# Kernel tuning notes

Hardware: AMD Instinct MI355X
Metric: run time of the kernel (lower is better)

## Reference

```python
import jax, jax.numpy as jnp
import numpy as np

D_MODEL = 1024
D_STATE = 8          # max(8, 16 // 2)
D_CONV = 4
D_INNER = int(1.5 * D_MODEL)   # expand = max(1.5, 2*0.75)
DT_RANK = (D_MODEL + 15) // 16 # 64
D_FF = 2 * D_MODEL
B, L = 2, 2048


def layer_norm(x, g, b, eps=1e-5):
    mu = jnp.mean(x, -1, keepdims=True)
    var = jnp.var(x, -1, keepdims=True)
    return (x - mu) * jax.lax.rsqrt(var + eps) * g + b


def setup_inputs() -> dict:
    key = jax.random.key(0)
    ks = jax.random.split(key, 12)
    def n(k, shape, scale=0.02):
        return jax.random.normal(k, shape, dtype=jnp.float32) * scale
    return {
        'x': jax.random.normal(ks[0], (B, L, D_MODEL), dtype=jnp.float32),
        'ln1_g': jnp.ones((D_MODEL,), jnp.float32),
        'ln1_b': jnp.zeros((D_MODEL,), jnp.float32),
        'ln2_g': jnp.ones((D_MODEL,), jnp.float32),
        'ln2_b': jnp.zeros((D_MODEL,), jnp.float32),
        'in_proj_w': n(ks[1], (2 * D_INNER, D_MODEL)),
        'conv_w': n(ks[2], (D_INNER, 1, D_CONV), 0.1),
        'conv_b': jnp.zeros((D_INNER,), jnp.float32),
        'x_proj_w': n(ks[3], (DT_RANK + 2 * D_STATE, D_INNER)),
        'dt_proj_w': n(ks[4], (D_INNER, DT_RANK), 0.1),
        'dt_proj_b': n(ks[5], (D_INNER,), 0.1),
        'A_log': jnp.log(jnp.broadcast_to(jnp.arange(1, D_STATE + 1, dtype=jnp.float32), (D_INNER, D_STATE))),
        'D': jnp.ones((D_INNER,), jnp.float32),
        'out_proj_w': n(ks[6], (D_MODEL, D_INNER)),
        'ffn_w1': n(ks[7], (D_FF, D_MODEL)),
        'ffn_b1': jnp.zeros((D_FF,), jnp.float32),
        'ffn_w2': n(ks[8], (D_MODEL, D_FF)),
        'ffn_b2': jnp.zeros((D_MODEL,), jnp.float32),
    }


def mamba(x, in_proj_w, conv_w, conv_b, x_proj_w, dt_proj_w, dt_proj_b, A_log, Dp, out_proj_w):
    # in_proj -> (x, z)
    xz = x @ in_proj_w.T                       # (B, L, 2*d_inner)
    xi, z = jnp.split(xz, 2, axis=-1)
    # depthwise causal conv over seq, kernel 4
    xc = jnp.transpose(xi, (0, 2, 1))          # (B, d_inner, L)
    xc = jax.lax.conv_general_dilated(
        xc, conv_w, window_strides=(1,), padding=[(D_CONV - 1, 0)],
        dimension_numbers=('NCH', 'OIH', 'NCH'), feature_group_count=D_INNER)
    xc = xc + conv_b[None, :, None]
    u = jax.nn.silu(jnp.transpose(xc, (0, 2, 1)))  # (B, L, d_inner)
    # x_proj -> dt, B, C
    x_dbl = u @ x_proj_w.T
    dt = x_dbl[..., :DT_RANK]
    Bm = x_dbl[..., DT_RANK:DT_RANK + D_STATE]
    Cm = x_dbl[..., DT_RANK + D_STATE:]
    delta = jax.nn.softplus(dt @ dt_proj_w.T + dt_proj_b)  # (B, L, d_inner)
    A = -jnp.exp(A_log)                                    # (d_inner, d_state)
    dA = jnp.exp(jnp.einsum('bld,dn->bldn', delta, A))     # (B, L, d_inner, d_state)
    dBu = jnp.einsum('bld,bln,bld->bldn', delta, Bm, u)
    # selective scan over time
    def step(h, inputs):
        dA_t, dBu_t, C_t = inputs
        h = dA_t * h + dBu_t                   # (B, d_inner, d_state)
        y = jnp.einsum('bdn,bn->bd', h, C_t)
        return h, y
    h0 = jnp.zeros((x.shape[0], D_INNER, D_STATE), x.dtype)
    _, ys = jax.lax.scan(step, h0, (jnp.moveaxis(dA, 1, 0), jnp.moveaxis(dBu, 1, 0), jnp.moveaxis(Cm, 1, 0)))
    y = jnp.moveaxis(ys, 0, 1) + u * Dp        # skip connection D*u
    y = y * jax.nn.silu(z)                     # gate
    return y @ out_proj_w.T


def reference(x, ln1_g, ln1_b, ln2_g, ln2_b, in_proj_w, conv_w, conv_b, x_proj_w,
              dt_proj_w, dt_proj_b, A_log, D, out_proj_w, ffn_w1, ffn_b1, ffn_w2, ffn_b2):
    residual = x
    xp = layer_norm(x, ln1_g, ln1_b)
    x = mamba(xp, in_proj_w, conv_w, conv_b, x_proj_w, dt_proj_w, dt_proj_b, A_log, D, out_proj_w) + residual
    xn = layer_norm(x, ln2_g, ln2_b)
    h = jax.nn.gelu(xn @ ffn_w1.T + ffn_b1, approximate=False)  # dropout is identity in eval
    return x + (h @ ffn_w2.T + ffn_b2)
```

## Files before the change

### kernel.cpp

```cpp
#include <hip/hip_runtime.h>
#include <math.h>

#define D_MODEL 1024
#define D_STATE 8
#define D_CONV  4
#define D_INNER 1536
#define DT_RANK 64
#define D_FF    2048
#define BATCH   2
#define SEQ     2048
#define NROWS   (BATCH*SEQ)
#define NC      32
#define LC      (SEQ/NC)
#define XPAD    128

typedef short bf16x8 __attribute__((ext_vector_type(8)));
typedef unsigned short u16x8 __attribute__((ext_vector_type(8)));
typedef float f32x4  __attribute__((ext_vector_type(4)));

__device__ inline unsigned short f2bf(float x) {
    union { float f; unsigned u; } v; v.f = x;
    unsigned r = v.u + 0x7fffu + ((v.u >> 16) & 1u);
    return (unsigned short)(r >> 16);
}
__device__ inline float bf2f(unsigned short h) {
    union { unsigned u; float f; } v; v.u = ((unsigned)h) << 16;
    return v.f;
}
__device__ inline float softplus_f(float x) {
    return (x > 20.0f) ? x : log1pf(__expf(x));
}
__device__ inline float gelu_f(float x) {
    return 0.5f * x * (1.0f + erff(x * 0.70710678118654752f));
}
__device__ inline float silu_f(float x) {
    return x / (1.0f + __expf(-x));
}
__device__ inline void gload16(const unsigned short* g, unsigned short* l) {
    typedef unsigned int u32;
    __builtin_amdgcn_global_load_lds(
        (const __attribute__((address_space(1))) u32*)g,
        (__attribute__((address_space(3))) u32*)l, 16, 0, 0);
}

#define PHASE_SYNC_PRE()  do { __builtin_amdgcn_s_barrier(); __builtin_amdgcn_sched_barrier(0); \
                               asm volatile("s_waitcnt lgkmcnt(0)" ::: "memory"); \
                               __builtin_amdgcn_sched_barrier(0); } while (0)
#define PHASE_SYNC_POST() do { __builtin_amdgcn_s_barrier(); __builtin_amdgcn_sched_barrier(0); } while (0)

__global__ __launch_bounds__(256) void wconv(const float* __restrict__ s0, unsigned short* __restrict__ d0,
                                             const float* __restrict__ s1, unsigned short* __restrict__ d1,
                                             const float* __restrict__ s2, unsigned short* __restrict__ d2,
                                             const float* __restrict__ s3, unsigned short* __restrict__ d3,
                                             const float* __restrict__ s4, unsigned short* __restrict__ d4) {
    int b = blockIdx.x;
    const float* s; unsigned short* d; int base;
    if      (b < 1536) { s = s0; d = d0; base = b * 2048; }
    else if (b < 1584) { s = s1; d = d1; base = (b - 1536) * 2048; }
    else if (b < 2352) { s = s2; d = d2; base = (b - 1584) * 2048; }
    else if (b < 3376) { s = s3; d = d3; base = (b - 2352) * 2048; }
    else               { s = s4; d = d4; base = (b - 3376) * 2048; }
    int i = base + threadIdx.x * 8;
    float4 v0 = *(const float4*)(s + i);
    float4 v1 = *(const float4*)(s + i + 4);
    ushort4 a, c;
    a.x = f2bf(v0.x); a.y = f2bf(v0.y); a.z = f2bf(v0.z); a.w = f2bf(v0.w);
    c.x = f2bf(v1.x); c.y = f2bf(v1.y); c.z = f2bf(v1.z); c.w = f2bf(v1.w);
    *(ushort4*)(d + i)     = a;
    *(ushort4*)(d + i + 4) = c;
}

__global__ __launch_bounds__(256) void xproj_pad(const float* __restrict__ src, unsigned short* __restrict__ dst) {
    int row = blockIdx.x;
    for (int c = threadIdx.x; c < D_INNER; c += 256)
        dst[row * D_INNER + c] = (row < 80) ? f2bf(src[row * D_INNER + c]) : (unsigned short)0;
}

__global__ __launch_bounds__(256) void ln_kernel(const float* __restrict__ x,
                                                 const float* __restrict__ g,
                                                 const float* __restrict__ b,
                                                 unsigned short* __restrict__ out) {
    __shared__ float sbuf[4];
    int row = blockIdx.x;
    int t = threadIdx.x;
    const float4* xr = (const float4*)(x + (size_t)row * D_MODEL);
    float4 v = xr[t];
    float s = v.x + v.y + v.z + v.w;
    for (int o = 32; o; o >>= 1) s += __shfl_down(s, o, 64);
    if ((t & 63) == 0) sbuf[t >> 6] = s;
    __syncthreads();
    float mu = (sbuf[0] + sbuf[1] + sbuf[2] + sbuf[3]) * (1.0f / D_MODEL);
    __syncthreads();
    float d0 = v.x - mu, d1 = v.y - mu, d2 = v.z - mu, d3 = v.w - mu;
    float q = d0*d0 + d1*d1 + d2*d2 + d3*d3;
    for (int o = 32; o; o >>= 1) q += __shfl_down(q, o, 64);
    if ((t & 63) == 0) sbuf[t >> 6] = q;
    __syncthreads();
    float var = (sbuf[0] + sbuf[1] + sbuf[2] + sbuf[3]) * (1.0f / D_MODEL);
    float rs = rsqrtf(var + 1e-5f);
    float4 gv = ((const float4*)g)[t];
    float4 bv = ((const float4*)b)[t];
    ushort4 st;
    st.x = f2bf(d0 * rs * gv.x + bv.x);
    st.y = f2bf(d1 * rs * gv.y + bv.y);
    st.z = f2bf(d2 * rs * gv.z + bv.z);
    st.w = f2bf(d3 * rs * gv.w + bv.w);
    ((ushort4*)(out + (size_t)row * D_MODEL))[t] = st;
}

#define EPI_F32        0
#define EPI_F32_BF16   1
#define EPI_SOFTPLUS   2
#define EPI_RESID      3
#define EPI_GELU_BF16  4
#define EPI_BIAS_RESID 5
#define EPI_BF16       6

template<int WN, int EPI>
__global__ __launch_bounds__(512, 2) void gemm8p(
    const unsigned short* __restrict__ A, int lda,
    const unsigned short* __restrict__ Bm, int ldb, int K,
    float* __restrict__ Cf, unsigned short* __restrict__ Cb, int ldc,
    const float* __restrict__ bias,
    const float* __restrict__ resid, int ldr) {
    constexpr int WM = 8 / WN;
    constexpr int BN = WN * 64;
    constexpr int RW = 256 / WM;
    constexpr int CW = 64;
    constexpr int MI = RW / 16;
    constexpr int NI = CW / 16;
    constexpr int MIH = MI / 2, NIH = NI / 2;
    constexpr int ABYTES = 256 * 128;
    constexpr int BBYTES = BN * 128;
    constexpr int BOFF = 2 * ABYTES;
    __shared__ unsigned short lds[(2 * ABYTES + 2 * BBYTES) / 2];

    const int t = threadIdx.x, l = t & 63, w = t >> 6;
    const int wr = w / WN, wc = w % WN;

    const int nx = gridDim.x;
    const int nwg = nx * gridDim.y;
    int bid = blockIdx.y * nx + blockIdx.x;
    int q = nwg >> 3;
    int swz = (bid & 7) * q + (bid >> 3);
    const int m0 = (swz / nx) * 256, n0 = (swz % nx) * BN;

    const int sr = l >> 3;
    const int sj = ((l & 7) * 16) ^ (((l >> 5) & 1) << 5);
    const int row_l = w * 8;
    const int row_c = (w >> 2) * 64 + (w & 3) * 8;

    auto STG = [&](int bufbyte, int rowbase, const unsigned short* G, int ldg, int gbase, int kt) {
        unsigned short* dst = (unsigned short*)((char*)lds + bufbyte + rowbase * 128);
        const unsigned short* src = G + (size_t)(gbase + rowbase + sr) * ldg + kt * 64 + (sj >> 1);
        gload16(src, dst);
    };
    auto S_Ah0 = [&](int b, int kt) {
        if (WN == 4) { STG(b * ABYTES, row_l, A, lda, m0, kt);       STG(b * ABYTES, 128 + row_l, A, lda, m0, kt); }
        else         { STG(b * ABYTES, row_c, A, lda, m0, kt);       STG(b * ABYTES, 128 + row_c, A, lda, m0, kt); }
    };
    auto S_Ah1 = [&](int b, int kt) {
        if (WN == 4) { STG(b * ABYTES, 64 + row_l, A, lda, m0, kt);  STG(b * ABYTES, 192 + row_l, A, lda, m0, kt); }
        else         { STG(b * ABYTES, 32 + row_c, A, lda, m0, kt);  STG(b * ABYTES, 160 + row_c, A, lda, m0, kt); }
    };
    auto S_Bc0 = [&](int b, int kt) {
        if (WN == 4) { STG(BOFF + b * BBYTES, row_c, Bm, ldb, n0, kt); STG(BOFF + b * BBYTES, 128 + row_c, Bm, ldb, n0, kt); }
        else         { STG(BOFF + b * BBYTES, row_c, Bm, ldb, n0, kt); }
    };
    auto S_Bc1 = [&](int b, int kt) {
        if (WN == 4) { STG(BOFF + b * BBYTES, 32 + row_c, Bm, ldb, n0, kt); STG(BOFF + b * BBYTES, 160 + row_c, Bm, ldb, n0, kt); }
        else         { STG(BOFF + b * BBYTES, 32 + row_c, Bm, ldb, n0, kt); }
    };

    auto LD = [&](int bytebase, int row, int kb) -> bf16x8 {
        int o = bytebase + row * 128 + (kb ^ (((row >> 2) & 1) << 5));
        return *(const bf16x8*)((const char*)lds + o);
    };

    f32x4 acc[MI][NI] = {};
    bf16x8 af[MIH][2], b0v[NIH][2], b1v[NIH][2];

    auto LDA_set = [&](int buf, int qr, auto& dst) {
        #pragma unroll
        for (int mi = 0; mi < MIH; mi++)
            #pragma unroll
            for (int ks = 0; ks < 2; ks++)
                dst[mi][ks] = LD(buf * ABYTES, wr * RW + qr * (RW / 2) + mi * 16 + (l & 15),
                                 ks * 64 + (l >> 4) * 16);
    };
    auto LDB_set = [&](int buf, int qc, auto& dst) {
        #pragma unroll
        for (int ni2 = 0; ni2 < NIH; ni2++)
            #pragma unroll
            for (int ks = 0; ks < 2; ks++)
                dst[ni2][ks] = LD(BOFF + buf * BBYTES, wc * CW + qc * 32 + ni2 * 16 + (l & 15),
                                  ks * 64 + (l >> 4) * 16);
    };
    auto MFMA_Q = [&](int qr, int qc, auto& a_, auto& b_) {
        __builtin_amdgcn_s_setprio(1);
        #pragma unroll
        for (int mi = 0; mi < MIH; mi++)
            #pragma unroll
            for (int ni2 = 0; ni2 < NIH; ni2++)
                #pragma unroll
                for (int ks = 0; ks < 2; ks++)
                    acc[qr * MIH + mi][qc * NIH + ni2] =
                        __builtin_amdgcn_mfma_f32_16x16x32_bf16(a_[mi][ks], b_[ni2][ks],
                                                                acc[qr * MIH + mi][qc * NIH + ni2], 0, 0, 0);
        __builtin_amdgcn_s_setprio(0);
    };
    auto VMW = [&](bool last) {
        if (last)            asm volatile("s_waitcnt vmcnt(0)" ::: "memory");
        else if (WN == 4)    asm volatile("s_waitcnt vmcnt(6)" ::: "memory");
        else                 asm volatile("s_waitcnt vmcnt(5)" ::: "memory");
        __builtin_amdgcn_sched_barrier(0);
    };

    const int ni_ = K >> 7;

    S_Ah0(0, 0); S_Ah1(0, 0); S_Bc0(0, 0); S_Bc1(0, 0);
    S_Ah0(1, 1); S_Ah1(1, 1); S_Bc0(1, 1); S_Bc1(1, 1);
    if (WN == 4) asm volatile("s_waitcnt vmcnt(8)" ::: "memory");
    else         asm volatile("s_waitcnt vmcnt(6)" ::: "memory");
    __builtin_amdgcn_s_barrier();
    __builtin_amdgcn_sched_barrier(0);

    for (int i = 0; i < ni_; i++) {
        const bool last = (i == ni_ - 1);
        const int t2 = 2 * i + 2, t3 = 2 * i + 3;
        LDA_set(0, 0, af); LDB_set(0, 0, b0v);
        if (i) S_Bc0(1, 2 * i + 1);
        PHASE_SYNC_PRE(); MFMA_Q(0, 0, af, b0v); PHASE_SYNC_POST();
        LDB_set(0, 1, b1v);
        if (!last) S_Ah0(0, t2);
        PHASE_SYNC_PRE(); MFMA_Q(0, 1, af, b1v); PHASE_SYNC_POST();
        LDA_set(0, 1, af);
        PHASE_SYNC_PRE(); MFMA_Q(1, 1, af, b1v); PHASE_SYNC_POST();
        LDB_set(0, 0, b0v);
        if (!last) { S_Ah1(0, t2); S_Bc1(0, t2); }
        VMW(last);
        PHASE_SYNC_PRE(); MFMA_Q(1, 0, af, b0v); PHASE_SYNC_POST();
        LDA_set(1, 0, af); LDB_set(1, 0, b0v);
        if (!last) S_Bc0(0, t2);
        PHASE_SYNC_PRE(); MFMA_Q(0, 0, af, b0v); PHASE_SYNC_POST();
        LDB_set(1, 1, b1v);
        if (!last) S_Ah0(1, t3);
        PHASE_SYNC_PRE(); MFMA_Q(0, 1, af, b1v); PHASE_SYNC_POST();
        LDA_set(1, 1, af);
        PHASE_SYNC_PRE(); MFMA_Q(1, 1, af, b1v); PHASE_SYNC_POST();
        LDB_set(1, 0, b0v);
        if (!last) { S_Ah1(1, t3); S_Bc1(1, t3); }
        VMW(last);
        PHASE_SYNC_PRE(); MFMA_Q(1, 0, af, b0v); PHASE_SYNC_POST();
    }

    #pragma unroll
    for (int ni2 = 0; ni2 < NI; ni2++) {
        int col = n0 + wc * CW + ni2 * 16 + (l & 15);
        float bv = 0.0f;
        if (EPI == EPI_SOFTPLUS || EPI == EPI_GELU_BF16 || EPI == EPI_BIAS_RESID) bv = bias[col];
        #pragma unroll
        for (int mi = 0; mi < MI; mi++) {
            #pragma unroll
            for (int j = 0; j < 4; j++) {
                int row = m0 + wr * RW + mi * 16 + (l >> 4) * 4 + j;
                float v = acc[mi][ni2][j];
                if (EPI == EPI_SOFTPLUS)        v = softplus_f(v + bv);
                else if (EPI == EPI_GELU_BF16)  v = gelu_f(v + bv);
                else if (EPI == EPI_RESID)      v = v + resid[(size_t)row * ldr + col];
                else if (EPI == EPI_BIAS_RESID) v = v + bv + resid[(size_t)row * ldr + col];
                if (EPI == EPI_GELU_BF16 || EPI == EPI_BF16) {
                    Cb[(size_t)row * ldc + col] = f2bf(v);
                } else {
                    Cf[(size_t)row * ldc + col] = v;
                    if (EPI == EPI_F32_BF16) Cb[(size_t)row * ldc + col] = f2bf(v);
                }
            }
        }
    }
}

template<int EPI, int SPLITK>
__global__ __launch_bounds__(256) void gemm_mfma(
    const unsigned short* __restrict__ A, int lda,
    const unsigned short* __restrict__ B, int ldb, int K,
    float* __restrict__ Cf, unsigned short* __restrict__ Cb, int ldc,
    const float* __restrict__ bias,
    const float* __restrict__ resid, int ldr) {
    __shared__ unsigned short As[3][128 * 32];
    __shared__ unsigned short Bs[3][128 * 32];
    int t = threadIdx.x, l = t & 63, w = t >> 6;
    int nx = gridDim.x;
    int nwg = nx * gridDim.y;
    int bid = blockIdx.y * nx + blockIdx.x;
    int q = nwg >> 3;
    int swz = (bid & 7) * q + (bid >> 3);
    int m0 = (swz / nx) * 128, n0 = (swz % nx) * 128;
    int kbase = (SPLITK > 1) ? blockIdx.z * K : 0;
    int c0 = 2 * w, c1 = 2 * w + 1;
    int srow = l >> 2, scol = (l & 3) * 8;
    const unsigned short* Ag0 = A + (size_t)(m0 + 16 * c0 + srow) * lda + kbase + scol;
    const unsigned short* Ag1 = A + (size_t)(m0 + 16 * c1 + srow) * lda + kbase + scol;
    const unsigned short* Bg0 = B + (size_t)(n0 + 16 * c0 + srow) * ldb + kbase + scol;
    const unsigned short* Bg1 = B + (size_t)(n0 + 16 * c1 + srow) * ldb + kbase + scol;
    int wr = w >> 1, wc = w & 1;
    int aoff = (wr * 64 + (l & 15)) * 32 + (l >> 4) * 8;
    int boff = (wc * 64 + (l & 15)) * 32 + (l >> 4) * 8;

    f32x4 acc[4][4] = {};
    int nt = K >> 5;

    gload16(Ag0, &As[0][c0 * 512]);
    gload16(Ag1, &As[0][c1 * 512]);
    gload16(Bg0, &Bs[0][c0 * 512]);
    gload16(Bg1, &Bs[0][c1 * 512]);
    if (nt > 1) {
        gload16(Ag0 + 32, &As[1][c0 * 512]);
        gload16(Ag1 + 32, &As[1][c1 * 512]);
        gload16(Bg0 + 32, &Bs[1][c0 * 512]);
        gload16(Bg1 + 32, &Bs[1][c1 * 512]);
    }

    int cur = 0;
    for (int ti = 0; ti < nt; ti++) {
        int pf = ti + 2;
        if (pf < nt) {
            int nb = cur - 1; if (nb < 0) nb += 3;
            int k0 = pf << 5;
            gload16(Ag0 + k0, &As[nb][c0 * 512]);
            gload16(Ag1 + k0, &As[nb][c1 * 512]);
            gload16(Bg0 + k0, &Bs[nb][c0 * 512]);
            gload16(Bg1 + k0, &Bs[nb][c1 * 512]);
        }
        int rem = nt - 1 - ti;
        if (rem >= 2)      asm volatile("s_waitcnt vmcnt(8)" ::: "memory");
        else if (rem == 1) asm volatile("s_waitcnt vmcnt(4)" ::: "memory");
        else               asm volatile("s_waitcnt vmcnt(0)" ::: "memory");
        __builtin_amdgcn_s_barrier();

        const unsigned short* Ab = &As[cur][0];
        const unsigned short* Bb = &Bs[cur][0];
        bf16x8 af[4], bfv[4];
        #pragma unroll
        for (int i = 0; i < 4; i++) af[i] = *(const bf16x8*)(Ab + aoff + i * 512);
        #pragma unroll
        for (int i = 0; i < 4; i++) bfv[i] = *(const bf16x8*)(Bb + boff + i * 512);
        __builtin_amdgcn_s_setprio(1);
        #pragma unroll
        for (int mi = 0; mi < 4; mi++)
            #pragma unroll
            for (int ni = 0; ni < 4; ni++)
                acc[mi][ni] = __builtin_amdgcn_mfma_f32_16x16x32_bf16(af[mi], bfv[ni], acc[mi][ni], 0, 0, 0);
        __builtin_amdgcn_s_setprio(0);
        __builtin_amdgcn_s_barrier();
        cur++; if (cur == 3) cur = 0;
    }

    if (SPLITK > 1) Cf += (size_t)blockIdx.z * NROWS * ldc;
    int colb = n0 + wc * 64 + (l & 15);
    int rowb = m0 + wr * 64 + (l >> 4) * 4;
    #pragma unroll
    for (int ni = 0; ni < 4; ni++) {
        int col = colb + ni * 16;
        float bv = 0.0f;
        if (EPI == EPI_SOFTPLUS || EPI == EPI_GELU_BF16 || EPI == EPI_BIAS_RESID) bv = bias[col];
        #pragma unroll
        for (int mi = 0; mi < 4; mi++) {
            #pragma unroll
            for (int j = 0; j < 4; j++) {
                int row = rowb + mi * 16 + j;
                float v = acc[mi][ni][j];
                if (EPI == EPI_SOFTPLUS)        v = softplus_f(v + bv);
                else if (EPI == EPI_GELU_BF16)  v = gelu_f(v + bv);
                else if (EPI == EPI_RESID)      v = v + resid[(size_t)row * ldr + col];
                else if (EPI == EPI_BIAS_RESID) v = v + bv + resid[(size_t)row * ldr + col];
                if (EPI == EPI_GELU_BF16 || EPI == EPI_BF16) {
                    Cb[(size_t)row * ldc + col] = f2bf(v);
                } else {
                    Cf[(size_t)row * ldc + col] = v;
                    if (EPI == EPI_F32_BF16) Cb[(size_t)row * ldc + col] = f2bf(v);
                }
            }
        }
    }
}

__global__ __launch_bounds__(256) void xdbl_reduce(const float* __restrict__ part,
                                                   float* __restrict__ xdbl,
                                                   unsigned short* __restrict__ xdbl_bf) {
    int i = blockIdx.x * 256 + threadIdx.x;
    const size_t seg = (size_t)NROWS * XPAD;
    float s = part[i] + part[i + seg] + part[i + 2 * seg] + part[i + 3 * seg];
    xdbl[i] = s;
    xdbl_bf[i] = f2bf(s);
}

__global__ __launch_bounds__(256) void conv_silu(const unsigned short* __restrict__ xz,
                                                 const float* __restrict__ w,
                                                 const float* __restrict__ cb,
                                                 unsigned short* __restrict__ u) {
    int idx = (blockIdx.x * 256 + threadIdx.x) * 8;
    int d = idx % D_INNER;
    int bl = idx / D_INNER;
    int l = bl & (SEQ - 1);
    float acc[8];
    float4 wv[8];
    #pragma unroll
    for (int j = 0; j < 8; j++) wv[j] = *(const float4*)(w + (d + j) * 4);
    float4 cb0 = *(const float4*)(cb + d);
    float4 cb1 = *(const float4*)(cb + d + 4);
    acc[0] = cb0.x; acc[1] = cb0.y; acc[2] = cb0.z; acc[3] = cb0.w;
    acc[4] = cb1.x; acc[5] = cb1.y; acc[6] = cb1.z; acc[7] = cb1.w;
    #pragma unroll
    for (int k = 0; k < 4; k++) {
        int lp = l - 3 + k;
        if (lp >= 0) {
            u16x8 s = *(const u16x8*)(xz + (size_t)(bl - 3 + k) * (2 * D_INNER) + d);
            #pragma unroll
            for (int j = 0; j < 8; j++) {
                float wk = (k == 0) ? wv[j].x : (k == 1) ? wv[j].y : (k == 2) ? wv[j].z : wv[j].w;
                acc[j] += bf2f((unsigned short)s[j]) * wk;
            }
        }
    }
    u16x8 o;
    #pragma unroll
    for (int j = 0; j < 8; j++) o[j] = f2bf(silu_f(acc[j]));
    *(u16x8*)(u + idx) = o;
}

__global__ __launch_bounds__(256) void scan_passA(const float* __restrict__ delta,
                                                  const unsigned short* __restrict__ u,
                                                  const float* __restrict__ xdbl,
                                                  const float* __restrict__ A_log,
                                                  float* __restrict__ P,
                                                  float* __restrict__ S) {
    int d = blockIdx.x * 256 + threadIdx.x;
    int c = blockIdx.y, b = blockIdx.z;
    __shared__ float bc[LC][16];
    int base_row = b * SEQ + c * LC;
    for (int e = threadIdx.x; e < LC * 16; e += 256) {
        int lrr = e >> 4, col = e & 15;
        bc[lrr][col] = xdbl[(size_t)(base_row + lrr) * XPAD + DT_RANK + col];
    }
    __syncthreads();
    float Ad[8];
    #pragma unroll
    for (int n = 0; n < 8; n++) Ad[n] = -__expf(A_log[d * 8 + n]);
    float prod[8], hs[8];
    #pragma unroll
    for (int n = 0; n < 8; n++) { prod[n] = 1.0f; hs[n] = 0.0f; }
    for (int lrr = 0; lrr < LC; lrr++) {
        int row = base_row + lrr;
        float dl = delta[(size_t)row * D_INNER + d];
        float uu = bf2f(u[(size_t)row * D_INNER + d]);
        float du = dl * uu;
        #pragma unroll
        for (int n = 0; n < 8; n++) {
            float dA = __expf(dl * Ad[n]);
            prod[n] *= dA;
            hs[n] = dA * hs[n] + du * bc[lrr][n];
        }
    }
    size_t o = ((size_t)((size_t)b * NC + c) * D_INNER + d) * 8;
    #pragma unroll
    for (int n = 0; n < 8; n++) { P[o + n] = prod[n]; S[o + n] = hs[n]; }
}

__global__ __launch_bounds__(256) void scan_passB(const float* __restrict__ P,
                                                  const float* __restrict__ S,
                                                  float* __restrict__ hstart) {
    int tid = blockIdx.x * 256 + threadIdx.x;
    int b = tid / (D_INNER * 8);
    int rem = tid % (D_INNER * 8);
    float h = 0.0f;
    for (int c = 0; c < NC; c++) {
        size_t o = (size_t)(b * NC + c) * (D_INNER * 8) + rem;
        hstart[o] = h;
        h = P[o] * h + S[o];
    }
}

__global__ __launch_bounds__(256) void scan_passC(const float* __restrict__ delta,
                                                  const unsigned short* __restrict__ u,
                                                  const float* __restrict__ xdbl,
                                                  const float* __restrict__ A_log,
                                                  const float* __restrict__ hstart,
                                                  const unsigned short* __restrict__ xz,
                                                  const float* __restrict__ Dp,
                                                  unsigned short* __restrict__ ygate) {
    int d = blockIdx.x * 256 + threadIdx.x;
    int c = blockIdx.y, b = blockIdx.z;
    __shared__ float bc[LC][16];
    int base_row = b * SEQ + c * LC;
    for (int e = threadIdx.x; e < LC * 16; e += 256) {
        int lrr = e >> 4, col = e & 15;
        bc[lrr][col] = xdbl[(size_t)(base_row + lrr) * XPAD + DT_RANK + col];
    }
    __syncthreads();
    float Ad[8];
    #pragma unroll
    for (int n = 0; n < 8; n++) Ad[n] = -__expf(A_log[d * 8 + n]);
    float h[8];
    size_t ho = ((size_t)((size_t)b * NC + c) * D_INNER + d) * 8;
    #pragma unroll
    for (int n = 0; n < 8; n++) h[n] = hstart[ho + n];
    float Dd = Dp[d];
    for (int lrr = 0; lrr < LC; lrr++) {
        int row = base_row + lrr;
        float dl = delta[(size_t)row * D_INNER + d];
        float uu = bf2f(u[(size_t)row * D_INNER + d]);
        float du = dl * uu;
        float y = 0.0f;
        #pragma unroll
        for (int n = 0; n < 8; n++) {
            float dA = __expf(dl * Ad[n]);
            h[n] = dA * h[n] + du * bc[lrr][n];
            y += h[n] * bc[lrr][8 + n];
        }
        y += uu * Dd;
        float z = bf2f(xz[(size_t)row * (2 * D_INNER) + D_INNER + d]);
        ygate[(size_t)row * D_INNER + d] = f2bf(y * silu_f(z));
    }
}

extern "C" void kernel_launch(void* const* d_in, const int* in_sizes, int n_in,
                              void* d_out, int out_size, void* d_ws, size_t ws_size,
                              hipStream_t stream) {
    const float* x         = (const float*)d_in[0];
    const float* ln1_g     = (const float*)d_in[1];
    const float* ln1_b     = (const float*)d_in[2];
    const float* ln2_g     = (const float*)d_in[3];
    const float* ln2_b     = (const float*)d_in[4];
    const float* in_proj_w = (const float*)d_in[5];
    const float* conv_w    = (const float*)d_in[6];
    const float* conv_b    = (const float*)d_in[7];
    const float* x_proj_w  = (const float*)d_in[8];
    const float* dt_proj_w = (const float*)d_in[9];
    const float* dt_proj_b = (const float*)d_in[10];
    const float* A_log     = (const float*)d_in[11];
    const float* Dp        = (const float*)d_in[12];
    const float* out_proj_w= (const float*)d_in[13];
    const float* ffn_w1    = (const float*)d_in[14];
    const float* ffn_b1    = (const float*)d_in[15];
    const float* ffn_w2    = (const float*)d_in[16];
    const float* ffn_b2    = (const float*)d_in[17];
    float* out = (float*)d_out;

    float* xdbl  = (float*)d_ws;
    float* delta = xdbl + (size_t)NROWS * XPAD;
    float* P     = delta + (size_t)NROWS * D_INNER;
    float* S     = P + (size_t)BATCH * NC * D_INNER * 8;
    float* hst   = S + (size_t)BATCH * NC * D_INNER * 8;
    float* x2    = hst + (size_t)BATCH * NC * D_INNER * 8;
    float* part  = x2;
    unsigned short* xz_bf   = (unsigned short*)(x2 + (size_t)NROWS * D_MODEL);
    unsigned short* xp_bf   = xz_bf + (size_t)NROWS * 2 * D_INNER;
    unsigned short* u_bf    = xp_bf + (size_t)NROWS * D_MODEL;
    unsigned short* xdbl_bf = u_bf + (size_t)NROWS * D_INNER;
    unsigned short* yg_bf   = xdbl_bf + (size_t)NROWS * XPAD;
    unsigned short* w_in    = yg_bf + (size_t)NROWS * D_INNER;
    unsigned short* w_xp    = w_in + (size_t)2 * D_INNER * D_MODEL;
    unsigned short* w_dt    = w_xp + (size_t)XPAD * D_INNER;
    unsigned short* w_out   = w_dt + (size_t)D_INNER * DT_RANK;
    unsigned short* w_f1    = w_out + (size_t)D_MODEL * D_INNER;
    unsigned short* w_f2    = w_f1 + (size_t)D_FF * D_MODEL;
    unsigned short* hff_bf  = xz_bf;

    wconv<<<4400, 256, 0, stream>>>(in_proj_w, w_in, dt_proj_w, w_dt, out_proj_w, w_out,
                                    ffn_w1, w_f1, ffn_w2, w_f2);
    xproj_pad<<<XPAD, 256, 0, stream>>>(x_proj_w, w_xp);
    ln_kernel<<<NROWS, 256, 0, stream>>>(x, ln1_g, ln1_b, xp_bf);
    gemm8p<4, EPI_BF16><<<dim3(3072 / 256, NROWS / 256), 512, 0, stream>>>(
        xp_bf, D_MODEL, w_in, D_MODEL, D_MODEL, nullptr, xz_bf, 2 * D_INNER, nullptr, nullptr, 0);
    conv_silu<<<(NROWS * D_INNER) / (256 * 8), 256, 0, stream>>>(xz_bf, conv_w, conv_b, u_bf);
    gemm_mfma<EPI_F32, 4><<<dim3(1, NROWS / 128, 4), 256, 0, stream>>>(
        u_bf, D_INNER, w_xp, D_INNER, D_INNER / 4, part, nullptr, XPAD, nullptr, nullptr, 0);
    xdbl_reduce<<<(NROWS * XPAD) / 256, 256, 0, stream>>>(part, xdbl, xdbl_bf);
    gemm_mfma<EPI_SOFTPLUS, 1><<<dim3(D_INNER / 128, NROWS / 128), 256, 0, stream>>>(
        xdbl_bf, XPAD, w_dt, DT_RANK, DT_RANK, delta, nullptr, D_INNER, dt_proj_b, nullptr, 0);
    scan_passA<<<dim3(D_INNER / 256, NC, BATCH), 256, 0, stream>>>(delta, u_bf, xdbl, A_log, P, S);
    scan_passB<<<(BATCH * D_INNER * 8) / 256, 256, 0, stream>>>(P, S, hst);
    scan_passC<<<dim3(D_INNER / 256, NC, BATCH), 256, 0, stream>>>(delta, u_bf, xdbl, A_log, hst, xz_bf, Dp, yg_bf);
    gemm8p<2, EPI_RESID><<<dim3(D_MODEL / 128, NROWS / 256), 512, 0, stream>>>(
        yg_bf, D_INNER, w_out, D_INNER, D_INNER, x2, nullptr, D_MODEL, nullptr, x, D_MODEL);
    ln_kernel<<<NROWS, 256, 0, stream>>>(x2, ln2_g, ln2_b, xp_bf);
    gemm8p<2, EPI_GELU_BF16><<<dim3(D_FF / 128, NROWS / 256), 512, 0, stream>>>(
        xp_bf, D_MODEL, w_f1, D_MODEL, D_MODEL, nullptr, hff_bf, D_FF, ffn_b1, nullptr, 0);
    gemm8p<2, EPI_BIAS_RESID><<<dim3(D_MODEL / 128, NROWS / 256), 512, 0, stream>>>(
        hff_bf, D_FF, w_f2, D_FF, D_FF, out, nullptr, D_MODEL, ffn_b2, x2, D_MODEL);
}
```

Before: 306.2 us.

## Split-K the out_proj and FFN2 GEMMs and change the LDS swizzle

The two N=1024 GEMMs (out_proj and ffn_w2) now run with split-K of 2 over a z grid dimension. Each writes fp32 partials into a scratch region that reuses the delta buffer, and a new vectorized reduce kernel adds the partials plus residual and optional bias. This doubles the workgroup count (from 128 to 256) so more CUs have work. The LDS XOR swizzle is also changed to a full 8-row pattern to reduce bank conflicts. The cost is an extra kernel launch and an extra round trip of partial sums through global memory.

```diff
diff --git a/kernel.cpp b/kernel.cpp
--- a/kernel.cpp
+++ b/kernel.cpp
@@ -116,7 +116,7 @@
 #define EPI_BIAS_RESID 5
 #define EPI_BF16       6
 
-template<int WN, int EPI>
+template<int WN, int EPI, int SPLITK>
 __global__ __launch_bounds__(512, 2) void gemm8p(
     const unsigned short* __restrict__ A, int lda,
     const unsigned short* __restrict__ Bm, int ldb, int K,
@@ -144,15 +144,16 @@
     int q = nwg >> 3;
     int swz = (bid & 7) * q + (bid >> 3);
     const int m0 = (swz / nx) * 256, n0 = (swz % nx) * BN;
+    const int kbase = (SPLITK > 1) ? blockIdx.z * K : 0;
 
     const int sr = l >> 3;
-    const int sj = ((l & 7) * 16) ^ (((l >> 5) & 1) << 5);
+    const int sj = ((l & 7) * 16) ^ ((l >> 3) << 4);
     const int row_l = w * 8;
     const int row_c = (w >> 2) * 64 + (w & 3) * 8;
 
     auto STG = [&](int bufbyte, int rowbase, const unsigned short* G, int ldg, int gbase, int kt) {
         unsigned short* dst = (unsigned short*)((char*)lds + bufbyte + rowbase * 128);
-        const unsigned short* src = G + (size_t)(gbase + rowbase + sr) * ldg + kt * 64 + (sj >> 1);
+        const unsigned short* src = G + (size_t)(gbase + rowbase + sr) * ldg + kbase + kt * 64 + (sj >> 1);
         gload16(src, dst);
     };
     auto S_Ah0 = [&](int b, int kt) {
@@ -173,7 +174,7 @@
     };
 
     auto LD = [&](int bytebase, int row, int kb) -> bf16x8 {
-        int o = bytebase + row * 128 + (kb ^ (((row >> 2) & 1) << 5));
+        int o = bytebase + row * 128 + (kb ^ ((row & 7) << 4));
         return *(const bf16x8*)((const char*)lds + o);
     };
 
@@ -254,6 +255,8 @@
         PHASE_SYNC_PRE(); MFMA_Q(1, 0, af, b0v); PHASE_SYNC_POST();
     }
 
+    float* Cfp = Cf;
+    if (SPLITK > 1) Cfp += (size_t)blockIdx.z * NROWS * ldc;
     #pragma unroll
     for (int ni2 = 0; ni2 < NI; ni2++) {
         int col = n0 + wc * CW + ni2 * 16 + (l & 15);
@@ -272,12 +275,38 @@
                 if (EPI == EPI_GELU_BF16 || EPI == EPI_BF16) {
                     Cb[(size_t)row * ldc + col] = f2bf(v);
                 } else {
-                    Cf[(size_t)row * ldc + col] = v;
+                    Cfp[(size_t)row * ldc + col] = v;
                     if (EPI == EPI_F32_BF16) Cb[(size_t)row * ldc + col] = f2bf(v);
                 }
             }
         }
     }
+}
+
+template<int WITH_BIAS>
+__global__ __launch_bounds__(256) void sk2_reduce(const float* __restrict__ p,
+                                                  const float* __restrict__ bias,
+                                                  const float* __restrict__ resid,
+                                                  float* __restrict__ o) {
+    int i = (blockIdx.x * 256 + threadIdx.x) * 4;
+    const size_t seg = (size_t)NROWS * D_MODEL;
+    float4 a = *(const float4*)(p + i);
+    float4 b = *(const float4*)(p + i + seg);
+    float4 r = *(const float4*)(resid + i);
+    float4 o4;
+    if (WITH_BIAS) {
+        float4 bb = *(const float4*)(bias + (i & (D_MODEL - 1)));
+        o4.x = a.x + b.x + r.x + bb.x;
+        o4.y = a.y + b.y + r.y + bb.y;
+        o4.z = a.z + b.z + r.z + bb.z;
+        o4.w = a.w + b.w + r.w + bb.w;
+    } else {
+        o4.x = a.x + b.x + r.x;
+        o4.y = a.y + b.y + r.y;
+        o4.z = a.z + b.z + r.z;
+        o4.w = a.w + b.w + r.w;
+    }
+    *(float4*)(o + i) = o4;
 }
 
 template<int EPI, int SPLITK>
@@ -554,6 +583,7 @@
     float* hst   = S + (size_t)BATCH * NC * D_INNER * 8;
     float* x2    = hst + (size_t)BATCH * NC * D_INNER * 8;
     float* part  = x2;
+    float* psum  = delta;
     unsigned short* xz_bf   = (unsigned short*)(x2 + (size_t)NROWS * D_MODEL);
     unsigned short* xp_bf   = xz_bf + (size_t)NROWS * 2 * D_INNER;
     unsigned short* u_bf    = xp_bf + (size_t)NROWS * D_MODEL;
@@ -571,7 +601,7 @@
                                     ffn_w1, w_f1, ffn_w2, w_f2);
     xproj_pad<<<XPAD, 256, 0, stream>>>(x_proj_w, w_xp);
     ln_kernel<<<NROWS, 256, 0, stream>>>(x, ln1_g, ln1_b, xp_bf);
-    gemm8p<4, EPI_BF16><<<dim3(3072 / 256, NROWS / 256), 512, 0, stream>>>(
+    gemm8p<4, EPI_BF16, 1><<<dim3(3072 / 256, NROWS / 256), 512, 0, stream>>>(
         xp_bf, D_MODEL, w_in, D_MODEL, D_MODEL, nullptr, xz_bf, 2 * D_INNER, nullptr, nullptr, 0);
     conv_silu<<<(NROWS * D_INNER) / (256 * 8), 256, 0, stream>>>(xz_bf, conv_w, conv_b, u_bf);
     gemm_mfma<EPI_F32, 4><<<dim3(1, NROWS / 128, 4), 256, 0, stream>>>(
@@ -582,11 +612,13 @@
     scan_passA<<<dim3(D_INNER / 256, NC, BATCH), 256, 0, stream>>>(delta, u_bf, xdbl, A_log, P, S);
     scan_passB<<<(BATCH * D_INNER * 8) / 256, 256, 0, stream>>>(P, S, hst);
     scan_passC<<<dim3(D_INNER / 256, NC, BATCH), 256, 0, stream>>>(delta, u_bf, xdbl, A_log, hst, xz_bf, Dp, yg_bf);
-    gemm8p<2, EPI_RESID><<<dim3(D_MODEL / 128, NROWS / 256), 512, 0, stream>>>(
-        yg_bf, D_INNER, w_out, D_INNER, D_INNER, x2, nullptr, D_MODEL, nullptr, x, D_MODEL);
+    gemm8p<2, EPI_F32, 2><<<dim3(D_MODEL / 128, NROWS / 256, 2), 512, 0, stream>>>(
+        yg_bf, D_INNER, w_out, D_INNER, D_INNER / 2, psum, nullptr, D_MODEL, nullptr, nullptr, 0);
+    sk2_reduce<0><<<(NROWS * D_MODEL) / 1024, 256, 0, stream>>>(psum, nullptr, x, x2);
     ln_kernel<<<NROWS, 256, 0, stream>>>(x2, ln2_g, ln2_b, xp_bf);
-    gemm8p<2, EPI_GELU_BF16><<<dim3(D_FF / 128, NROWS / 256), 512, 0, stream>>>(
+    gemm8p<2, EPI_GELU_BF16, 1><<<dim3(D_FF / 128, NROWS / 256), 512, 0, stream>>>(
         xp_bf, D_MODEL, w_f1, D_MODEL, D_MODEL, nullptr, hff_bf, D_FF, ffn_b1, nullptr, 0);
-    gemm8p<2, EPI_BIAS_RESID><<<dim3(D_MODEL / 128, NROWS / 256), 512, 0, stream>>>(
-        hff_bf, D_FF, w_f2, D_FF, D_FF, out, nullptr, D_MODEL, ffn_b2, x2, D_MODEL);
-}
+    gemm8p<2, EPI_F32, 2><<<dim3(D_MODEL / 128, NROWS / 256, 2), 512, 0, stream>>>(
+        hff_bf, D_FF, w_f2, D_FF, D_FF / 2, psum, nullptr, D_MODEL, nullptr, nullptr, 0);
+    sk2_reduce<1><<<(NROWS * D_MODEL) / 1024, 256, 0, stream>>>(psum, ffn_b2, x2, out);
+}
```

New measurement: 290.4 us. 5.2% less time.
